# Kernel tuning notes

Hardware: AMD Instinct MI355X
Metric: run time of the kernel (lower is better)

Reference implementation:

```python
import jax, jax.numpy as jnp
import numpy as np

B, N, D = 2, 2048, 1024
H, DH = 16, 64
DEPTH = 4
FF = 4
EPS = 1e-3  # keras LayerNormalization default epsilon
SCALE = DH ** -0.5


def setup_inputs() -> dict:
    key = jax.random.key(0)
    ks = jax.random.split(key, 8)
    s = 0.02
    inner = H * DH
    return {
        "x": jax.random.normal(ks[0], (B, N, D), jnp.float32),
        "mask": jnp.ones((B, N), jnp.bool_),
        "ln1_g": jnp.ones((DEPTH, D), jnp.float32),
        "ln1_b": jnp.zeros((DEPTH, D), jnp.float32),
        "Wqkv": jax.random.normal(ks[1], (DEPTH, D, 3 * inner), jnp.float32) * s,
        "Wout": jax.random.normal(ks[2], (DEPTH, inner, D), jnp.float32) * s,
        "bout": jnp.zeros((DEPTH, D), jnp.float32),
        "ln2_g": jnp.ones((DEPTH, D), jnp.float32),
        "ln2_b": jnp.zeros((DEPTH, D), jnp.float32),
        "W1": jax.random.normal(ks[3], (DEPTH, D, 2 * FF * D), jnp.float32) * s,
        "b1": jnp.zeros((DEPTH, 2 * FF * D), jnp.float32),
        "W2": jax.random.normal(ks[4], (DEPTH, FF * D, D), jnp.float32) * s,
        "b2": jnp.zeros((DEPTH, D), jnp.float32),
    }


def _layernorm(x, g, b):
    mu = jnp.mean(x, axis=-1, keepdims=True)
    var = jnp.mean(jnp.square(x - mu), axis=-1, keepdims=True)
    return (x - mu) * jax.lax.rsqrt(var + EPS) * g + b


def _attention(x, mask, Wqkv, Wout, bout):
    b, n, _ = x.shape
    qkv = x @ Wqkv  # [b, n, 3*h*dh]
    q, k, v = jnp.split(qkv, 3, axis=-1)
    split_heads = lambda t: t.reshape(b, n, H, DH).transpose(0, 2, 1, 3)  # b h n d
    q, k, v = split_heads(q), split_heads(k), split_heads(v)
    dots = jnp.einsum("bhid,bhjd->bhij", q, k) * SCALE
    neg = -jnp.finfo(dots.dtype).max
    # padding mask: keep (i valid) & (j valid)
    pm = mask[:, None, :, None] & mask[:, None, None, :]
    dots = jnp.where(pm, dots, neg)
    # causal mask: strict upper triangle masked out (triu with k=1)
    causal = jnp.triu(jnp.ones((n, n), jnp.bool_), k=1)
    dots = jnp.where(causal, neg, dots)
    attn = jax.nn.softmax(dots, axis=-1)
    out = jnp.einsum("bhij,bhjd->bhid", attn, v)
    out = out.transpose(0, 2, 1, 3).reshape(b, n, H * DH)
    return out @ Wout + bout


def _feedforward(x, W1, b1, W2, b2):
    h = x @ W1 + b1
    a, gates = jnp.split(h, 2, axis=-1)
    h = a * jax.nn.gelu(gates, approximate=False)  # GEGLU, tf.nn.gelu exact
    return h @ W2 + b2


def reference(x, mask, ln1_g, ln1_b, Wqkv, Wout, bout, ln2_g, ln2_b, W1, b1, W2, b2):
    for l in range(DEPTH):
        x = x + _attention(_layernorm(x, ln1_g[l], ln1_b[l]), mask, Wqkv[l], Wout[l], bout[l])
        x = x + _feedforward(_layernorm(x, ln2_g[l], ln2_b[l]), W1[l], b1[l], W2[l], b2[l])
    return x
```

## Files before the change

kernel.cpp:

```cpp
#include <hip/hip_runtime.h>


typedef float f32x4 __attribute__((ext_vector_type(4)));
typedef __bf16 bf16x8 __attribute__((ext_vector_type(8)));
typedef unsigned short u16;
typedef unsigned int u32;

#define SCALE2 0.18033688011112042f
#define LN_EPS 1e-3f
#define DEFER_THR 8.0f

__device__ __forceinline__ float fexp2(float x) { return __builtin_amdgcn_exp2f(x); }

__device__ __forceinline__ u16 f2bf(float f) {
  u32 u = __float_as_uint(f);
  u += 0x7fffu + ((u >> 16) & 1u);
  return (u16)(u >> 16);
}

__device__ __forceinline__ void stage16(void* lds_wave_base, const void* gsrc) {
  __builtin_amdgcn_global_load_lds((__attribute__((address_space(1))) void*)gsrc,
                                   (__attribute__((address_space(3))) void*)lds_wave_base,
                                   16, 0, 0);
}

__global__ void wtrans_kernel(const float* __restrict__ W, u16* __restrict__ WT,
                              int K, int N, int permMode) {
  __shared__ float tile[32][33];
  const int n0 = blockIdx.x * 32, k0 = blockIdx.y * 32;
  const float* Wl = W + (size_t)blockIdx.z * K * N;
  u16* WTl = WT + (size_t)blockIdx.z * K * N;
  const int tx = threadIdx.x, ty = threadIdx.y;
#pragma unroll
  for (int i = 0; i < 4; ++i)
    tile[ty + i * 8][tx] = Wl[(size_t)(k0 + ty + i * 8) * N + n0 + tx];
  __syncthreads();
#pragma unroll
  for (int i = 0; i < 4; ++i) {
    const int n = n0 + ty + i * 8;
    int orow;
    if (permMode) {
      orow = (n < 4096) ? (((n >> 4) << 5) + (n & 15))
                        : ((((n - 4096) >> 4) << 5) + 16 + (n & 15));
    } else {
      orow = n;
    }
    WTl[(size_t)orow * K + k0 + tx] = f2bf(tile[tx][ty + i * 8]);
  }
}

__global__ void vtrans_kernel(const u16* __restrict__ qkv, u16* __restrict__ Vt) {
  __shared__ u16 tile[32][33];
  const int t0 = blockIdx.x * 32, d0 = blockIdx.y * 32, bh = blockIdx.z;
  const int b = bh >> 4, h = bh & 15;
  const int tx = threadIdx.x, ty = threadIdx.y;
#pragma unroll
  for (int i = 0; i < 4; ++i)
    tile[ty + i * 8][tx] =
        qkv[((size_t)(b * 2048 + t0 + ty + i * 8)) * 3072 + 2048 + h * 64 + d0 + tx];
  __syncthreads();
#pragma unroll
  for (int i = 0; i < 4; ++i)
    Vt[((size_t)bh * 64 + d0 + ty + i * 8) * 2048 + t0 + tx] = tile[tx][ty + i * 8];
}

__global__ __launch_bounds__(256, 4)
void ln_kernel(const float* __restrict__ x, const float* __restrict__ g,
               const float* __restrict__ b, u16* __restrict__ y) {
  const int row = blockIdx.x, tid = threadIdx.x;
  const float4 v = ((const float4*)(x + (size_t)row * 1024))[tid];
  float s = v.x + v.y + v.z + v.w;
  float s2 = v.x * v.x + v.y * v.y + v.z * v.z + v.w * v.w;
#pragma unroll
  for (int off = 32; off > 0; off >>= 1) {
    s += __shfl_down(s, off);
    s2 += __shfl_down(s2, off);
  }
  __shared__ float ps[8];
  __shared__ float stats[2];
  const int wv = tid >> 6, lane = tid & 63;
  if (lane == 0) { ps[wv] = s; ps[wv + 4] = s2; }
  __syncthreads();
  if (tid == 0) {
    const float S = ps[0] + ps[1] + ps[2] + ps[3];
    const float S2 = ps[4] + ps[5] + ps[6] + ps[7];
    const float mu = S * (1.0f / 1024.0f);
    const float var = S2 * (1.0f / 1024.0f) - mu * mu;
    stats[0] = mu;
    stats[1] = rsqrtf(var + LN_EPS);
  }
  __syncthreads();
  const float mu = stats[0], rs = stats[1];
  const float4 gg = ((const float4*)g)[tid];
  const float4 bb = ((const float4*)b)[tid];
  ushort4 ov;
  ov.x = f2bf((v.x - mu) * rs * gg.x + bb.x);
  ov.y = f2bf((v.y - mu) * rs * gg.y + bb.y);
  ov.z = f2bf((v.z - mu) * rs * gg.z + bb.z);
  ov.w = f2bf((v.w - mu) * rs * gg.w + bb.w);
  ((ushort4*)(y + (size_t)row * 1024))[tid] = ov;
}

template <int EPI>
__global__ __launch_bounds__(512, 2)
void gemm5(const u16* __restrict__ A, const u16* __restrict__ B,
           float* __restrict__ resid, const float* __restrict__ bias,
           u16* __restrict__ out, int M, int N, int K) {
  __shared__ __align__(16) u16 lds[2][4][256 * 32];

  const int tid = threadIdx.x;
  const int wv = tid >> 6, lane = tid & 63;
  const int lr = lane & 15, lg = lane >> 4;
  const int wmi = wv >> 2, wni = wv & 3;
  const int RB0 = wmi * 128, CB0 = wni * 64;

  const int nwg = (int)(gridDim.x * gridDim.y);
  int id = (int)(blockIdx.y * gridDim.x + blockIdx.x);
  id = (id & 7) * (nwg >> 3) + (id >> 3);
  const int m0 = (id / (int)gridDim.x) * 256, n0 = (id % (int)gridDim.x) * 256;

  auto stageHalf = [&](int c, int reg, int k0) {
    const u16* src = (reg < 2) ? A : B;
    const int base0 = (reg < 2) ? m0 : n0;
    const int h = reg & 1;
#pragma unroll
    for (int l = 0; l < 2; ++l) {
      const int o = l * 8192 + wv * 1024;
      const int lo = o + lane * 16;
      const int row = lo >> 6;
      const int c16 = (lo >> 4) & 3;
      stage16((char*)&lds[c][reg][0] + o,
              src + (size_t)(base0 + row) * K + k0 + h * 32 + c16 * 8);
    }
  };

  f32x4 acc[8][4] = {};
  bf16x8 afr[4], bfr[4];

  const int nT = K >> 6;
  stageHalf(0, 0, 0); stageHalf(0, 2, 0); stageHalf(0, 1, 0); stageHalf(0, 3, 0);
  asm volatile("s_waitcnt vmcnt(4)\n\ts_barrier" ::: "memory");

  for (int t = 0; t < nT; ++t) {
    const int c = t & 1, oc = c ^ 1;
    const bool nxt = (t + 1 < nT);
    const int k1 = (t + 1) * 64;
    const char* Ak0 = (const char*)&lds[c][0][0];
    const char* Ak1 = (const char*)&lds[c][1][0];
    const char* Bk0 = (const char*)&lds[c][2][0];
    const char* Bk1 = (const char*)&lds[c][3][0];

#pragma unroll
    for (int i = 0; i < 4; ++i)
      afr[i] = *(const bf16x8*)(Ak0 + (RB0 + i * 16 + lr) * 64 + lg * 16);
#pragma unroll
    for (int j = 0; j < 4; ++j)
      bfr[j] = *(const bf16x8*)(Bk0 + (CB0 + j * 16 + lr) * 64 + lg * 16);
    if (nxt) stageHalf(oc, 0, k1);
    asm volatile("s_barrier" ::: "memory");
    asm volatile("s_waitcnt lgkmcnt(0)" ::: "memory");
    __builtin_amdgcn_sched_barrier(0);
    __builtin_amdgcn_s_setprio(1);
#pragma unroll
    for (int i = 0; i < 4; ++i)
#pragma unroll
      for (int j = 0; j < 4; ++j)
        acc[i][j] = __builtin_amdgcn_mfma_f32_16x16x32_bf16(afr[i], bfr[j], acc[i][j], 0, 0, 0);
    __builtin_amdgcn_s_setprio(0);
    asm volatile("s_barrier" ::: "memory");

#pragma unroll
    for (int i = 0; i < 4; ++i)
      afr[i] = *(const bf16x8*)(Ak0 + (RB0 + (4 + i) * 16 + lr) * 64 + lg * 16);
    if (nxt) stageHalf(oc, 2, k1);
    asm volatile("s_barrier" ::: "memory");
    asm volatile("s_waitcnt lgkmcnt(0)" ::: "memory");
    __builtin_amdgcn_sched_barrier(0);
    __builtin_amdgcn_s_setprio(1);
#pragma unroll
    for (int i = 0; i < 4; ++i)
#pragma unroll
      for (int j = 0; j < 4; ++j)
        acc[4 + i][j] = __builtin_amdgcn_mfma_f32_16x16x32_bf16(afr[i], bfr[j], acc[4 + i][j], 0, 0, 0);
    __builtin_amdgcn_s_setprio(0);
    if (nxt) asm volatile("s_waitcnt vmcnt(4)\n\ts_barrier" ::: "memory");
    else     asm volatile("s_waitcnt vmcnt(0)\n\ts_barrier" ::: "memory");

#pragma unroll
    for (int i = 0; i < 4; ++i)
      afr[i] = *(const bf16x8*)(Ak1 + (RB0 + (4 + i) * 16 + lr) * 64 + lg * 16);
#pragma unroll
    for (int j = 0; j < 4; ++j)
      bfr[j] = *(const bf16x8*)(Bk1 + (CB0 + j * 16 + lr) * 64 + lg * 16);
    if (nxt) stageHalf(oc, 1, k1);
    asm volatile("s_barrier" ::: "memory");
    asm volatile("s_waitcnt lgkmcnt(0)" ::: "memory");
    __builtin_amdgcn_sched_barrier(0);
    __builtin_amdgcn_s_setprio(1);
#pragma unroll
    for (int i = 0; i < 4; ++i)
#pragma unroll
      for (int j = 0; j < 4; ++j)
        acc[4 + i][j] = __builtin_amdgcn_mfma_f32_16x16x32_bf16(afr[i], bfr[j], acc[4 + i][j], 0, 0, 0);
    __builtin_amdgcn_s_setprio(0);
    asm volatile("s_barrier" ::: "memory");

#pragma unroll
    for (int i = 0; i < 4; ++i)
      afr[i] = *(const bf16x8*)(Ak1 + (RB0 + i * 16 + lr) * 64 + lg * 16);
    if (nxt) stageHalf(oc, 3, k1);
    asm volatile("s_barrier" ::: "memory");
    asm volatile("s_waitcnt lgkmcnt(0)" ::: "memory");
    __builtin_amdgcn_sched_barrier(0);
    __builtin_amdgcn_s_setprio(1);
#pragma unroll
    for (int i = 0; i < 4; ++i)
#pragma unroll
      for (int j = 0; j < 4; ++j)
        acc[i][j] = __builtin_amdgcn_mfma_f32_16x16x32_bf16(afr[i], bfr[j], acc[i][j], 0, 0, 0);
    __builtin_amdgcn_s_setprio(0);
    if (nxt) asm volatile("s_waitcnt vmcnt(4)\n\ts_barrier" ::: "memory");
  }

  if (EPI == 0) {
#pragma unroll
    for (int mt = 0; mt < 8; ++mt)
#pragma unroll
      for (int nt = 0; nt < 4; ++nt) {
        const int n = n0 + CB0 + nt * 16 + lr;
#pragma unroll
        for (int r = 0; r < 4; ++r) {
          const int m = m0 + RB0 + mt * 16 + lg * 4 + r;
          out[(size_t)m * N + n] = f2bf(acc[mt][nt][r]);
        }
      }
  } else {
#pragma unroll
    for (int pt = 0; pt < 2; ++pt) {
      const int colA = ((n0 + CB0 + pt * 32) >> 5) * 16 + lr;
      const float ba = bias[colA];
      const float bg = bias[4096 + colA];
#pragma unroll
      for (int mt = 0; mt < 8; ++mt)
#pragma unroll
        for (int r = 0; r < 4; ++r) {
          const int m = m0 + RB0 + mt * 16 + lg * 4 + r;
          const float a = acc[mt][2 * pt][r] + ba;
          const float g = acc[mt][2 * pt + 1][r] + bg;
          const float gl = 0.5f * g * (1.0f + erff(g * 0.70710678118654752f));
          out[(size_t)m * 4096 + colA] = f2bf(a * gl);
        }
    }
  }
}

template <int EPI, int BM, int BN, int WM, int WN>
__global__ __launch_bounds__(WM * WN * 64, 2)
void gemm4(const u16* __restrict__ A, const u16* __restrict__ B,
           float* __restrict__ resid, const float* __restrict__ bias,
           u16* __restrict__ out, int M, int N, int K) {
  constexpr int NTHR = WM * WN * 64;
  constexpr int MT = BM / WM / 16;
  constexpr int NT = BN / WN / 16;
  __shared__ __align__(16) u16 lds[2][(BM + BN) * 64];

  const int tid = threadIdx.x;
  const int wv = tid >> 6, lane = tid & 63;
  const int lr = lane & 15, lg = lane >> 4;
  const int wmi = wv / WN, wni = wv % WN;
  const int RB0 = wmi * (BM / WM), CB0 = wni * (BN / WN);

  const int nwg = (int)(gridDim.x * gridDim.y);
  int id = (int)(blockIdx.y * gridDim.x + blockIdx.x);
  id = (id & 7) * (nwg >> 3) + (id >> 3);
  const int m0 = (id / (int)gridDim.x) * BM, n0 = (id % (int)gridDim.x) * BN;

  auto stage = [&](int bsel, int k0) {
    u16* dstA = &lds[bsel][0];
    u16* dstB = &lds[bsel][BM * 64];
#pragma unroll
    for (int rnd = 0; rnd < (BM * 128) / (NTHR * 16); ++rnd) {
      const int base = rnd * (NTHR * 16) + wv * 1024;
      const int off = base + lane * 16;
      const int row = off >> 7;
      const int k2 = (off & 127) ^ ((row & 7) << 4);
      stage16((char*)dstA + base, A + (size_t)(m0 + row) * K + k0 + (k2 >> 1));
    }
#pragma unroll
    for (int rnd = 0; rnd < (BN * 128) / (NTHR * 16); ++rnd) {
      const int base = rnd * (NTHR * 16) + wv * 1024;
      const int off = base + lane * 16;
      const int row = off >> 7;
      const int k2 = (off & 127) ^ ((row & 7) << 4);
      stage16((char*)dstB + base, B + (size_t)(n0 + row) * K + k0 + (k2 >> 1));
    }
  };

  f32x4 acc[MT][NT] = {};
  bf16x8 afr0[MT], bfr0[NT], afr1[MT], bfr1[NT];

  auto rd = [&](int bsel, int ks, bf16x8 (&af)[MT], bf16x8 (&bf)[NT]) {
    const char* As = (const char*)&lds[bsel][0];
    const char* Bs = (const char*)&lds[bsel][BM * 64];
#pragma unroll
    for (int mt = 0; mt < MT; ++mt) {
      const int row = RB0 + mt * 16 + lr;
      af[mt] = *(const bf16x8*)(As + row * 128 + ((ks * 64 + lg * 16) ^ ((lr & 7) << 4)));
    }
#pragma unroll
    for (int nt = 0; nt < NT; ++nt) {
      const int row = CB0 + nt * 16 + lr;
      bf[nt] = *(const bf16x8*)(Bs + row * 128 + ((ks * 64 + lg * 16) ^ ((lr & 7) << 4)));
    }
  };

  const int nT = K >> 6;
  stage(0, 0);
  stage(1, 64);
  asm volatile("s_waitcnt vmcnt(8)\n\ts_barrier" ::: "memory");
  rd(0, 0, afr0, bfr0);
  __builtin_amdgcn_sched_barrier(0);

  for (int t = 0; t < nT; ++t) {
    const int c = t & 1;
    rd(c, 1, afr1, bfr1);
    __builtin_amdgcn_sched_barrier(0);
    __builtin_amdgcn_s_setprio(1);
#pragma unroll
    for (int mt = 0; mt < MT; ++mt)
#pragma unroll
      for (int nt = 0; nt < NT; ++nt)
        acc[mt][nt] = __builtin_amdgcn_mfma_f32_16x16x32_bf16(
            afr0[mt], bfr0[nt], acc[mt][nt], 0, 0, 0);
    __builtin_amdgcn_s_setprio(0);
    __builtin_amdgcn_sched_barrier(0);
    asm volatile("s_waitcnt lgkmcnt(0)\n\ts_barrier" ::: "memory");
    __builtin_amdgcn_sched_barrier(0);
    if (t + 2 < nT) stage(c, (t + 2) * 64);
    if (t + 1 < nT) {
      if (t + 2 < nT)
        asm volatile("s_waitcnt vmcnt(8)\n\ts_barrier" ::: "memory");
      else
        asm volatile("s_waitcnt vmcnt(0)\n\ts_barrier" ::: "memory");
      rd(c ^ 1, 0, afr0, bfr0);
      __builtin_amdgcn_sched_barrier(0);
    }
    __builtin_amdgcn_s_setprio(1);
#pragma unroll
    for (int mt = 0; mt < MT; ++mt)
#pragma unroll
      for (int nt = 0; nt < NT; ++nt)
        acc[mt][nt] = __builtin_amdgcn_mfma_f32_16x16x32_bf16(
            afr1[mt], bfr1[nt], acc[mt][nt], 0, 0, 0);
    __builtin_amdgcn_s_setprio(0);
  }

  if (EPI == 1) {
    float bs[NT];
#pragma unroll
    for (int nt = 0; nt < NT; ++nt) bs[nt] = bias[n0 + CB0 + nt * 16 + lr];
#pragma unroll
    for (int mt = 0; mt < MT; ++mt)
#pragma unroll
      for (int nt = 0; nt < NT; ++nt) {
        const int n = n0 + CB0 + nt * 16 + lr;
#pragma unroll
        for (int r = 0; r < 4; ++r) {
          const int m = m0 + RB0 + mt * 16 + lg * 4 + r;
          resid[(size_t)m * N + n] += acc[mt][nt][r] + bs[nt];
        }
      }
  } else {
#pragma unroll
    for (int mt = 0; mt < MT; ++mt)
#pragma unroll
      for (int nt = 0; nt < NT; ++nt) {
        const int n = n0 + CB0 + nt * 16 + lr;
#pragma unroll
        for (int r = 0; r < 4; ++r) {
          const int m = m0 + RB0 + mt * 16 + lg * 4 + r;
          out[(size_t)m * N + n] = f2bf(acc[mt][nt][r]);
        }
      }
  }
}

__global__ __launch_bounds__(512, 4)
void attn_kernel(const u16* __restrict__ qkv, const u16* __restrict__ Vt,
                 u16* __restrict__ attnout) {
  __shared__ __align__(16) u16 KV[2][2][64 * 64];
  __shared__ __align__(16) u16 Ps[8][16 * 64];

  const int tid = threadIdx.x;
  const int wv = tid >> 6, lane = tid & 63;
  const int lr = lane & 15, lg = lane >> 4;
  const int lin = (int)(blockIdx.y * gridDim.x + blockIdx.x);
  const int xcd = lin & 7, j = lin >> 3;
  const int bh = xcd * 4 + (j >> 4);
  const int pr = j & 15;
  const int b = bh >> 4, h = bh & 15;
  const size_t tokbase = (size_t)b * 2048;
  const int qhi = 31 - pr;
  const int qt = (wv < 4) ? qhi : pr;
  const int ws = wv & 3;
  const int qg = qt * 64 + ws * 16 + lr;

  bf16x8 qf[2];
#pragma unroll
  for (int ks = 0; ks < 2; ++ks)
    qf[ks] = *(const bf16x8*)(qkv + (tokbase + qt * 64 + ws * 16 + lr) * 3072 +
                              h * 64 + ks * 32 + lg * 8);

  f32x4 o[4] = {};
  float m = -1e30f, lp = 0.f;

  const u16* kg_base = qkv + tokbase * 3072 + 1024 + h * 64;
  const u16* vg_base = Vt + (size_t)bh * 64 * 2048;

  const int soff = tid * 16;
  const int srow = soff >> 7;
  const int scol = (soff & 127) ^ ((srow & 7) << 4);
  auto stage = [&](int bsel, int kt2) {
    stage16((char*)&KV[bsel][0][0] + wv * 1024,
            kg_base + (size_t)(kt2 * 64 + srow) * 3072 + (scol >> 1));
    stage16((char*)&KV[bsel][1][0] + wv * 1024,
            vg_base + (size_t)srow * 2048 + kt2 * 64 + (scol >> 1));
  };

  stage(0, 0);
  stage(1, 1);
  asm volatile("s_waitcnt vmcnt(2)\n\ts_barrier" ::: "memory");

  for (int kt = 0; kt <= qhi; ++kt) {
    if (kt <= qt) {
      const char* Ks = (const char*)&KV[kt & 1][0][0];
      const char* Vs = (const char*)&KV[kt & 1][1][0];

      f32x4 s[4] = {};
#pragma unroll
      for (int ks = 0; ks < 2; ++ks)
#pragma unroll
        for (int nt = 0; nt < 4; ++nt) {
          const int row = nt * 16 + lr;
          const bf16x8 kf = *(const bf16x8*)(Ks + row * 128 +
                                             ((ks * 64 + lg * 16) ^ ((lr & 7) << 4)));
          s[nt] = __builtin_amdgcn_mfma_f32_16x16x32_bf16(kf, qf[ks], s[nt], 0, 0, 0);
        }

      float pmax = -1e30f;
      const bool diag = (kt == qt);
#pragma unroll
      for (int nt = 0; nt < 4; ++nt)
#pragma unroll
        for (int r = 0; r < 4; ++r) {
          float v = s[nt][r] * SCALE2;
          if (diag) {
            const int kg = kt * 64 + nt * 16 + lg * 4 + r;
            v = (kg <= qg) ? v : -1e30f;
          }
          s[nt][r] = v;
          pmax = fmaxf(pmax, v);
        }

      if (!__all(pmax - m <= DEFER_THR)) {
        float mx = fmaxf(pmax, __shfl_xor(pmax, 16));
        mx = fmaxf(mx, __shfl_xor(mx, 32));
        const float mn = fmaxf(m, mx);
        const float alpha = fexp2(m - mn);
        m = mn;
        lp *= alpha;
#pragma unroll
        for (int r = 0; r < 4; ++r) {
          const float ar = __shfl(alpha, lg * 4 + r);
#pragma unroll
          for (int dt = 0; dt < 4; ++dt) o[dt][r] *= ar;
        }
      }

#pragma unroll
      for (int nt = 0; nt < 4; ++nt) {
        const float p0 = fexp2(s[nt][0] - m), p1 = fexp2(s[nt][1] - m);
        const float p2 = fexp2(s[nt][2] - m), p3 = fexp2(s[nt][3] - m);
        lp += (p0 + p1) + (p2 + p3);
        uint2 w;
        w.x = (u32)f2bf(p0) | ((u32)f2bf(p1) << 16);
        w.y = (u32)f2bf(p2) | ((u32)f2bf(p3) << 16);
        *(uint2*)((char*)&Ps[wv][0] + lr * 128 + ((nt * 32 + lg * 8) ^ ((lr & 7) << 4))) = w;
      }

      bf16x8 pf[2];
#pragma unroll
      for (int ks = 0; ks < 2; ++ks) {
        const int jp = (ks * 4 + lg) ^ (lr & 7);
        pf[ks] = *(const bf16x8*)(&Ps[wv][0] + lr * 64 + jp * 8);
      }
#pragma unroll
      for (int ks = 0; ks < 2; ++ks)
#pragma unroll
        for (int dt = 0; dt < 4; ++dt) {
          const int row = dt * 16 + lr;
          const bf16x8 vf = *(const bf16x8*)(Vs + row * 128 +
                                             ((ks * 64 + lg * 16) ^ ((lr & 7) << 4)));
          o[dt] = __builtin_amdgcn_mfma_f32_16x16x32_bf16(pf[ks], vf, o[dt], 0, 0, 0);
        }
    }

    __syncthreads();
    if (kt + 2 <= qhi) stage(kt & 1, kt + 2);
    asm volatile("s_barrier" ::: "memory");
  }

  float lsum = lp + __shfl_xor(lp, 16);
  lsum += __shfl_xor(lsum, 32);
#pragma unroll
  for (int r = 0; r < 4; ++r) {
    const float ld = __shfl(lsum, lg * 4 + r);
    const int tok = qt * 64 + ws * 16 + lg * 4 + r;
#pragma unroll
    for (int dt = 0; dt < 4; ++dt)
      attnout[(tokbase + tok) * 1024 + h * 64 + dt * 16 + lr] = f2bf(o[dt][r] / ld);
  }
}

extern "C" void kernel_launch(void* const* d_in, const int* in_sizes, int n_in,
                              void* d_out, int out_size, void* d_ws, size_t ws_size,
                              hipStream_t stream) {
  (void)in_sizes; (void)n_in; (void)ws_size;
  const float* x_in  = (const float*)d_in[0];
  const float* ln1_g = (const float*)d_in[2];
  const float* ln1_b = (const float*)d_in[3];
  const float* Wqkv  = (const float*)d_in[4];
  const float* Wout  = (const float*)d_in[5];
  const float* bout  = (const float*)d_in[6];
  const float* ln2_g = (const float*)d_in[7];
  const float* ln2_b = (const float*)d_in[8];
  const float* W1    = (const float*)d_in[9];
  const float* b1    = (const float*)d_in[10];
  const float* W2    = (const float*)d_in[11];
  const float* b2    = (const float*)d_in[12];
  float* x = (float*)d_out;

  char* ws = (char*)d_ws;
  size_t off = 0;
  auto alloc = [&](size_t bytes) -> void* {
    void* p = ws + off;
    off += (bytes + 255) & ~(size_t)255;
    return p;
  };
  u16* WqkvT = (u16*)alloc(4ull * 3072 * 1024 * 2);
  u16* WoutT = (u16*)alloc(4ull * 1024 * 1024 * 2);
  u16* W1T   = (u16*)alloc(4ull * 8192 * 1024 * 2);
  u16* W2T   = (u16*)alloc(4ull * 1024 * 4096 * 2);
  u16* y     = (u16*)alloc(4096ull * 1024 * 2);
  u16* qkvb  = (u16*)alloc(4096ull * 3072 * 2);
  u16* Vt    = (u16*)alloc(32ull * 64 * 2048 * 2);
  u16* attn  = (u16*)alloc(4096ull * 1024 * 2);
  u16* ff    = (u16*)alloc(4096ull * 4096 * 2);

  hipMemcpyAsync(x, x_in, (size_t)out_size * 4, hipMemcpyDeviceToDevice, stream);

  const dim3 tb(32, 8);
  wtrans_kernel<<<dim3(3072 / 32, 1024 / 32, 4), tb, 0, stream>>>(Wqkv, WqkvT, 1024, 3072, 0);
  wtrans_kernel<<<dim3(1024 / 32, 1024 / 32, 4), tb, 0, stream>>>(Wout, WoutT, 1024, 1024, 0);
  wtrans_kernel<<<dim3(8192 / 32, 1024 / 32, 4), tb, 0, stream>>>(W1, W1T, 1024, 8192, 1);
  wtrans_kernel<<<dim3(1024 / 32, 4096 / 32, 4), tb, 0, stream>>>(W2, W2T, 4096, 1024, 0);

  for (int l = 0; l < 4; ++l) {
    ln_kernel<<<4096, 256, 0, stream>>>(x, ln1_g + l * 1024, ln1_b + l * 1024, y);
    gemm5<0><<<dim3(3072 / 256, 4096 / 256), 512, 0, stream>>>(
        y, WqkvT + (size_t)l * 3072 * 1024, nullptr, nullptr, qkvb, 4096, 3072, 1024);
    vtrans_kernel<<<dim3(64, 2, 32), tb, 0, stream>>>(qkvb, Vt);
    attn_kernel<<<dim3(16, 32), 512, 0, stream>>>(qkvb, Vt, attn);
    gemm4<1, 128, 128, 2, 2><<<dim3(1024 / 128, 4096 / 128), 256, 0, stream>>>(
        attn, WoutT + (size_t)l * 1024 * 1024, x, bout + l * 1024, nullptr, 4096, 1024, 1024);
    ln_kernel<<<4096, 256, 0, stream>>>(x, ln2_g + l * 1024, ln2_b + l * 1024, y);
    gemm5<2><<<dim3(8192 / 256, 4096 / 256), 512, 0, stream>>>(
        y, W1T + (size_t)l * 8192 * 1024, nullptr, b1 + l * 8192, ff, 4096, 8192, 1024);
    gemm4<1, 128, 128, 2, 2><<<dim3(1024 / 128, 4096 / 128), 256, 0, stream>>>(
        ff, W2T + (size_t)l * 1024 * 4096, x, b2 + l * 1024, nullptr, 4096, 1024, 4096);
  }
}
```

Baseline: 1.208 ms.

## Restructure gemm5 LDS layout with XOR swizzle and deeper A prefetch; use gemm4 for QKV

The gemm5 shared-memory layout changes from four 32-wide K halves to one 64-wide K row per A/B tile. Reads and async global-to-LDS stores use an XOR swizzle to avoid bank conflicts. The staging schedule is reordered so A chunks for tile t+2 load during the last compute phase, while B chunks for t+1 stream in earlier, aiming to hide more global-memory latency. The QKV projection moves from gemm5 to the 128x128 gemm4 kernel, which raises workgroup count for that GEMM but gives up the larger tile's data reuse. The two-ahead prefetch into the buffer still being read depends on exact barrier placement, a possible race risk.

```diff
diff --git a/kernel.cpp b/kernel.cpp
--- a/kernel.cpp
+++ b/kernel.cpp
@@ -106,7 +106,7 @@
 void gemm5(const u16* __restrict__ A, const u16* __restrict__ B,
            float* __restrict__ resid, const float* __restrict__ bias,
            u16* __restrict__ out, int M, int N, int K) {
-  __shared__ __align__(16) u16 lds[2][4][256 * 32];
+  __shared__ __align__(16) u16 lds[2][512 * 64];
 
   const int tid = threadIdx.x;
   const int wv = tid >> 6, lane = tid & 63;
@@ -119,44 +119,54 @@
   id = (id & 7) * (nwg >> 3) + (id >> 3);
   const int m0 = (id / (int)gridDim.x) * 256, n0 = (id % (int)gridDim.x) * 256;
 
-  auto stageHalf = [&](int c, int reg, int k0) {
-    const u16* src = (reg < 2) ? A : B;
-    const int base0 = (reg < 2) ? m0 : n0;
-    const int h = reg & 1;
+  auto stageChunk = [&](int bsel, int ch, int k0) {
+    const u16* src = (ch < 2) ? A : B;
+    const int rbase = (ch < 2) ? m0 : n0;
+    u16* dst = &lds[bsel][(ch < 2) ? 0 : 256 * 64];
+    const int rh = (ch & 1) * 128;
 #pragma unroll
     for (int l = 0; l < 2; ++l) {
-      const int o = l * 8192 + wv * 1024;
-      const int lo = o + lane * 16;
-      const int row = lo >> 6;
-      const int c16 = (lo >> 4) & 3;
-      stage16((char*)&lds[c][reg][0] + o,
-              src + (size_t)(base0 + row) * K + k0 + h * 32 + c16 * 8);
+      const int base = rh * 128 + l * 8192 + wv * 1024;
+      const int off = base + lane * 16;
+      const int row = off >> 7;
+      const int k2 = (off & 127) ^ ((row & 7) << 4);
+      stage16((char*)dst + base, src + (size_t)(rbase + row) * K + k0 + (k2 >> 1));
     }
   };
 
   f32x4 acc[8][4] = {};
   bf16x8 afr[4], bfr[4];
 
+  auto rdA = [&](const char* As, int ks, int mh) {
+#pragma unroll
+    for (int i = 0; i < 4; ++i) {
+      const int row = RB0 + mh * 64 + i * 16 + lr;
+      afr[i] = *(const bf16x8*)(As + row * 128 +
+                                ((ks * 64 + lg * 16) ^ ((lr & 7) << 4)));
+    }
+  };
+  auto rdB = [&](const char* Bs, int ks) {
+#pragma unroll
+    for (int j = 0; j < 4; ++j) {
+      const int row = CB0 + j * 16 + lr;
+      bfr[j] = *(const bf16x8*)(Bs + row * 128 +
+                                ((ks * 64 + lg * 16) ^ ((lr & 7) << 4)));
+    }
+  };
+
   const int nT = K >> 6;
-  stageHalf(0, 0, 0); stageHalf(0, 2, 0); stageHalf(0, 1, 0); stageHalf(0, 3, 0);
+  stageChunk(0, 0, 0); stageChunk(0, 1, 0); stageChunk(0, 2, 0); stageChunk(0, 3, 0);
+  stageChunk(1, 0, 64); stageChunk(1, 1, 64);
   asm volatile("s_waitcnt vmcnt(4)\n\ts_barrier" ::: "memory");
 
   for (int t = 0; t < nT; ++t) {
     const int c = t & 1, oc = c ^ 1;
-    const bool nxt = (t + 1 < nT);
-    const int k1 = (t + 1) * 64;
-    const char* Ak0 = (const char*)&lds[c][0][0];
-    const char* Ak1 = (const char*)&lds[c][1][0];
-    const char* Bk0 = (const char*)&lds[c][2][0];
-    const char* Bk1 = (const char*)&lds[c][3][0];
-
-#pragma unroll
-    for (int i = 0; i < 4; ++i)
-      afr[i] = *(const bf16x8*)(Ak0 + (RB0 + i * 16 + lr) * 64 + lg * 16);
-#pragma unroll
-    for (int j = 0; j < 4; ++j)
-      bfr[j] = *(const bf16x8*)(Bk0 + (CB0 + j * 16 + lr) * 64 + lg * 16);
-    if (nxt) stageHalf(oc, 0, k1);
+    const char* As = (const char*)&lds[c][0];
+    const char* Bs = (const char*)&lds[c][256 * 64];
+    const int k1 = (t + 1) * 64, k2t = (t + 2) * 64;
+
+    rdA(As, 0, 0); rdB(Bs, 0);
+    if (t + 1 < nT) stageChunk(oc, 2, k1);
     asm volatile("s_barrier" ::: "memory");
     asm volatile("s_waitcnt lgkmcnt(0)" ::: "memory");
     __builtin_amdgcn_sched_barrier(0);
@@ -169,10 +179,8 @@
     __builtin_amdgcn_s_setprio(0);
     asm volatile("s_barrier" ::: "memory");
 
-#pragma unroll
-    for (int i = 0; i < 4; ++i)
-      afr[i] = *(const bf16x8*)(Ak0 + (RB0 + (4 + i) * 16 + lr) * 64 + lg * 16);
-    if (nxt) stageHalf(oc, 2, k1);
+    rdA(As, 0, 1);
+    if (t + 1 < nT) stageChunk(oc, 3, k1);
     asm volatile("s_barrier" ::: "memory");
     asm volatile("s_waitcnt lgkmcnt(0)" ::: "memory");
     __builtin_amdgcn_sched_barrier(0);
@@ -183,16 +191,9 @@
       for (int j = 0; j < 4; ++j)
         acc[4 + i][j] = __builtin_amdgcn_mfma_f32_16x16x32_bf16(afr[i], bfr[j], acc[4 + i][j], 0, 0, 0);
     __builtin_amdgcn_s_setprio(0);
-    if (nxt) asm volatile("s_waitcnt vmcnt(4)\n\ts_barrier" ::: "memory");
-    else     asm volatile("s_waitcnt vmcnt(0)\n\ts_barrier" ::: "memory");
-
-#pragma unroll
-    for (int i = 0; i < 4; ++i)
-      afr[i] = *(const bf16x8*)(Ak1 + (RB0 + (4 + i) * 16 + lr) * 64 + lg * 16);
-#pragma unroll
-    for (int j = 0; j < 4; ++j)
-      bfr[j] = *(const bf16x8*)(Bk1 + (CB0 + j * 16 + lr) * 64 + lg * 16);
-    if (nxt) stageHalf(oc, 1, k1);
+    asm volatile("s_barrier" ::: "memory");
+
+    rdA(As, 1, 1); rdB(Bs, 1);
     asm volatile("s_barrier" ::: "memory");
     asm volatile("s_waitcnt lgkmcnt(0)" ::: "memory");
     __builtin_amdgcn_sched_barrier(0);
@@ -205,12 +206,11 @@
     __builtin_amdgcn_s_setprio(0);
     asm volatile("s_barrier" ::: "memory");
 
-#pragma unroll
-    for (int i = 0; i < 4; ++i)
-      afr[i] = *(const bf16x8*)(Ak1 + (RB0 + i * 16 + lr) * 64 + lg * 16);
-    if (nxt) stageHalf(oc, 3, k1);
-    asm volatile("s_barrier" ::: "memory");
+    rdA(As, 1, 0);
     asm volatile("s_waitcnt lgkmcnt(0)" ::: "memory");
+    __builtin_amdgcn_sched_barrier(0);
+    asm volatile("s_barrier" ::: "memory");
+    if (t + 2 < nT) { stageChunk(c, 0, k2t); stageChunk(c, 1, k2t); }
     __builtin_amdgcn_sched_barrier(0);
     __builtin_amdgcn_s_setprio(1);
 #pragma unroll
@@ -219,7 +219,12 @@
       for (int j = 0; j < 4; ++j)
         acc[i][j] = __builtin_amdgcn_mfma_f32_16x16x32_bf16(afr[i], bfr[j], acc[i][j], 0, 0, 0);
     __builtin_amdgcn_s_setprio(0);
-    if (nxt) asm volatile("s_waitcnt vmcnt(4)\n\ts_barrier" ::: "memory");
+    if (t + 1 < nT) {
+      if (t + 2 < nT)
+        asm volatile("s_waitcnt vmcnt(4)\n\ts_barrier" ::: "memory");
+      else
+        asm volatile("s_waitcnt vmcnt(0)\n\ts_barrier" ::: "memory");
+    }
   }
 
   if (EPI == 0) {
@@ -567,7 +572,7 @@
 
   for (int l = 0; l < 4; ++l) {
     ln_kernel<<<4096, 256, 0, stream>>>(x, ln1_g + l * 1024, ln1_b + l * 1024, y);
-    gemm5<0><<<dim3(3072 / 256, 4096 / 256), 512, 0, stream>>>(
+    gemm4<0, 128, 128, 2, 2><<<dim3(3072 / 128, 4096 / 128), 256, 0, stream>>>(
         y, WqkvT + (size_t)l * 3072 * 1024, nullptr, nullptr, qkvb, 4096, 3072, 1024);
     vtrans_kernel<<<dim3(64, 2, 32), tb, 0, stream>>>(qkvb, Vt);
     attn_kernel<<<dim3(16, 32), 512, 0, stream>>>(qkvb, Vt, attn);
```

Measured after the change: 1.170 ms. 1.03x faster.
